# Performance work log

Hardware: AMD Instinct MI355X
Metric: run time of the kernel (lower is better)

The kernel has to match this reference:

```python
import jax, jax.numpy as jnp
import numpy as np

A, B, S, ADIM = 8, 8192, 128, 16   # n_agents, batch, state_dim, act_dim
H, HEADS = 512, 4                   # hidc, att_heads
D = H // HEADS                      # att_dim
EPS = 1e-5


def _ln(x):
    # LayerNorm over last dim, no affine (elementwise_affine=False), eps=1e-5
    m = jnp.mean(x, axis=-1, keepdims=True)
    v = jnp.var(x, axis=-1, keepdims=True)
    return (x - m) * jax.lax.rsqrt(v + EPS)


def setup_inputs() -> dict:
    key = jax.random.key(0)
    ks = jax.random.split(key, 16)
    sc = 0.02
    return {
        "states": jax.random.normal(ks[0], (A, B, S), jnp.float32),
        "actions": jax.random.normal(ks[1], (A, B, ADIM), jnp.float32),
        # per-agent state encoders (Encoder built with hidc in the source)
        "Ws_s": jax.random.normal(ks[2], (A, S, H), jnp.float32) * sc,
        "bs_s": jnp.zeros((A, H), jnp.float32),
        # per-agent state-action encoders
        "Ws_sa": jax.random.normal(ks[3], (A, S + ADIM, H), jnp.float32) * sc,
        "bs_sa": jnp.zeros((A, H), jnp.float32),
        # shared per-head key/value/selector projections
        "Wk": jax.random.normal(ks[4], (HEADS, H, D), jnp.float32) * sc,
        "Wv": jax.random.normal(ks[5], (HEADS, H, D), jnp.float32) * sc,
        "Wsel": jax.random.normal(ks[6], (HEADS, H, D), jnp.float32) * sc,
        "bsel": jnp.zeros((HEADS, D), jnp.float32),
        # per-agent critics: Linear(2H -> H), LeakyReLU, Linear(H -> ADIM)
        "Wc1": jax.random.normal(ks[7], (A, 2 * H, H), jnp.float32) * sc,
        "bc1": jnp.zeros((A, H), jnp.float32),
        "Wc2": jax.random.normal(ks[8], (A, H, ADIM), jnp.float32) * sc,
        "bc2": jnp.zeros((A, ADIM), jnp.float32),
    }


def reference(states, actions, Ws_s, bs_s, Ws_sa, bs_sa,
              Wk, Wv, Wsel, bsel, Wc1, bc1, Wc2, bc2):
    lrelu = jax.nn.leaky_relu  # slope 0.01 matches torch default

    # per-agent state encodings: [A,B,H]
    s_enc = lrelu(jnp.einsum('abs,ash->abh', _ln(states), Ws_s) + bs_s[:, None, :])

    # per-agent state-action encodings: [A,B,H]
    sa = jnp.concatenate([states, actions], axis=-1)
    sa_enc = lrelu(jnp.einsum('abs,ash->abh', _ln(sa), Ws_sa) + bs_sa[:, None, :])

    # per-head keys / values / selectors: [HEADS, A, B, D]
    keys = jnp.einsum('abh,khd->kabd', sa_enc, Wk)
    vals = jnp.einsum('abh,khd->kabd', sa_enc, Wv)
    sel = lrelu(jnp.einsum('abh,khd->kabd', sa_enc, Wsel) + bsel[:, None, None, :])

    # attention logits of agent i over agents j != i: [HEADS, A, A, B]
    logits = jnp.einsum('kibd,kjbd->kijb', sel, keys) / np.sqrt(D).astype(np.float32)
    self_mask = jnp.eye(A, dtype=bool)[None, :, :, None]
    w = jax.nn.softmax(jnp.where(self_mask, -jnp.inf, logits), axis=2)

    # attended values: [HEADS, A, B, D] -> concat heads -> [A, B, H]
    qvals = jnp.einsum('kijb,kjbd->kibd', w, vals)
    values = qvals.transpose(1, 2, 0, 3).reshape(A, B, H)

    # per-agent critics on concat(state_enc, attended values)
    cin = jnp.concatenate([s_enc, values], axis=-1)           # [A,B,2H]
    h1 = lrelu(jnp.einsum('abf,afh->abh', _ln(cin), Wc1) + bc1[:, None, :])
    all_qs = jnp.einsum('abh,aho->abo', h1, Wc2) + bc2[:, None, :]  # [A,B,ADIM]

    # Q of taken (argmax) action per agent: [A,B,1]
    idx = jnp.argmax(actions, axis=-1)
    q = jnp.take_along_axis(all_qs, idx[..., None], axis=-1)
    return q
```

## Files before the change

kernel.cpp:

```cpp
#include <hip/hip_runtime.h>
#include <hip/hip_bf16.h>
#include <math.h>


#define AN 8
#define BNB 8192
#define SN 128
#define ADN 16
#define HN 512
#define NHEADS 4
#define DN 128

typedef __hip_bfloat16 bf16;
typedef unsigned short u16;
typedef __attribute__((ext_vector_type(8))) short bf16x8;
typedef __attribute__((ext_vector_type(4))) float f32x4;

__device__ __forceinline__ float lrelu(float x){ return x > 0.f ? x : 0.01f*x; }
__device__ __forceinline__ float bflo(unsigned u){ return __uint_as_float(u << 16); }
__device__ __forceinline__ float bfhi(unsigned u){ return __uint_as_float(u & 0xffff0000u); }
__device__ __forceinline__ float bf2f(u16 u){ return __uint_as_float((unsigned)u << 16); }
__device__ __forceinline__ u16 f2bf(float v){
  union { bf16 h; u16 s; } cv; cv.h = __float2bfloat16(v); return cv.s;
}
__device__ __forceinline__ ushort4 f4bf(float4 v){
  ushort4 u; u.x=f2bf(v.x); u.y=f2bf(v.y); u.z=f2bf(v.z); u.w=f2bf(v.w); return u;
}

__device__ __forceinline__ void gload16(const u16* g, u16* l){
  __builtin_amdgcn_global_load_lds(
      (const __attribute__((address_space(1))) unsigned int*)(g),
      (__attribute__((address_space(3))) unsigned int*)(l), 16, 0, 0);
}

__global__ __launch_bounds__(256) void prep_kernel(
    const float* __restrict__ states, const float* __restrict__ actions,
    u16* __restrict__ sa_bf, float2* __restrict__ st_s, float2* __restrict__ st_sa,
    int* __restrict__ aip)
{
  const int lane = threadIdx.x & 63;
  const int r = blockIdx.x*4 + (threadIdx.x >> 6);
  float2 sv = ((const float2*)(states + (size_t)r*SN))[lane];
  float s1 = sv.x + sv.y, q1 = sv.x*sv.x + sv.y*sv.y;
  float2 av = make_float2(0.f, 0.f);
  if (lane < 8) av = ((const float2*)(actions + (size_t)r*ADN))[lane];
  float s2 = s1 + av.x + av.y, q2 = q1 + av.x*av.x + av.y*av.y;
  #pragma unroll
  for (int off=32; off; off>>=1){
    s1 += __shfl_xor(s1,off); q1 += __shfl_xor(q1,off);
    s2 += __shfl_xor(s2,off); q2 += __shfl_xor(q2,off);
  }
  float bv; int bi;
  if (lane < 8){
    if (av.x >= av.y){ bv = av.x; bi = 2*lane; } else { bv = av.y; bi = 2*lane+1; }
  } else { bv = -INFINITY; bi = 999; }
  #pragma unroll
  for (int off=1; off<8; off<<=1){
    float ov = __shfl_xor(bv, off); int oi = __shfl_xor(bi, off);
    if (ov > bv || (ov == bv && oi < bi)){ bv = ov; bi = oi; }
  }
  u16* row = sa_bf + (size_t)r*192;
  ushort2 p; p.x = f2bf(sv.x); p.y = f2bf(sv.y);
  *(ushort2*)(row + 2*lane) = p;
  if (lane < 8){
    ushort2 pa; pa.x = f2bf(av.x); pa.y = f2bf(av.y);
    *(ushort2*)(row + 128 + 2*lane) = pa;
  } else if (lane < 32){
    ushort2 z; z.x = 0; z.y = 0;
    *(ushort2*)(row + 128 + 2*lane) = z;
  }
  if (lane==0){
    float m1 = s1*(1.f/128.f), v1 = fmaxf(q1*(1.f/128.f)-m1*m1, 0.f);
    st_s[r] = make_float2(m1, rsqrtf(v1+1e-5f));
    float m2 = s2*(1.f/144.f), v2 = fmaxf(q2*(1.f/144.f)-m2*m2, 0.f);
    st_sa[r] = make_float2(m2, rsqrtf(v2+1e-5f));
    aip[r] = bi;
  }
}

__global__ __launch_bounds__(256) void transw_all_kernel(
    const float* __restrict__ Ws_s, const float* __restrict__ Ws_sa, const float* __restrict__ Wc1,
    const float* __restrict__ Wk, const float* __restrict__ Wv, const float* __restrict__ Wsel,
    u16* __restrict__ Wt_s, u16* __restrict__ Wt_sa, u16* __restrict__ Wt_c1, u16* __restrict__ Wt_p)
{
  __shared__ float t[32][33];
  int id = blockIdx.x;
  const float* in; u16* outp; int K, Kp; size_t zs; int gx;
  const int N = (id < 5376) ? 512 : 128;
  if (id < 512){            in=Ws_s;  outp=Wt_s;            K=128;  Kp=128;  zs=(size_t)512*128;  gx=4;  }
  else if (id < 1280){ id-=512;  in=Ws_sa; outp=Wt_sa;      K=144;  Kp=192;  zs=(size_t)512*192;  gx=6;  }
  else if (id < 5376){ id-=1280; in=Wc1;   outp=Wt_c1;      K=1024; Kp=1024; zs=(size_t)512*1024; gx=32; }
  else if (id < 5632){ id-=5376; in=Wk;    outp=Wt_p;            K=512; Kp=512; zs=(size_t)3*128*512; gx=16; }
  else if (id < 5888){ id-=5632; in=Wv;    outp=Wt_p+128*512;    K=512; Kp=512; zs=(size_t)3*128*512; gx=16; }
  else {               id-=5888; in=Wsel;  outp=Wt_p+2*128*512;  K=512; Kp=512; zs=(size_t)3*128*512; gx=16; }
  const int bx = id % gx; id /= gx;
  const int gy = N >> 5;
  const int by = id % gy;
  const int z  = id / gy;
  const int tx = threadIdx.x, ty = threadIdx.y;
  const int k0 = bx*32, n0 = by*32;
  const float* ip = in + (size_t)z*K*N;
  #pragma unroll
  for (int i=0;i<4;i++){
    int k = k0 + ty*4 + i;
    t[ty*4+i][tx] = (k < K) ? ip[(size_t)k*N + n0 + tx] : 0.f;
  }
  __syncthreads();
  u16* op = outp + (size_t)z*zs;
  #pragma unroll
  for (int i=0;i<4;i++){
    int n = n0 + ty*4 + i;
    op[(size_t)n*Kp + k0 + tx] = f2bf(t[tx][ty*4+i]);
  }
}

__global__ __launch_bounds__(256) void colsum_bf_kernel(
    const u16* __restrict__ Wt_s, const u16* __restrict__ Wt_sa, const u16* __restrict__ Wt_c1,
    float* __restrict__ cs_s, float* __restrict__ cs_sa, float* __restrict__ cs_c1)
{
  const int lane = threadIdx.x & 63;
  const int row = blockIdx.x*4 + (threadIdx.x >> 6);
  const int which = row >> 12; const int idx = row & 4095;
  const u16* W; int K; float* outp;
  if (which==0){ W = Wt_s;  K = 128;  outp = cs_s;  }
  else if (which==1){ W = Wt_sa; K = 192;  outp = cs_sa; }
  else { W = Wt_c1; K = 1024; outp = cs_c1; }
  const u16* p = W + (size_t)idx*K;
  float s = 0.f;
  for (int c = lane*8; c < K; c += 512){
    uint4 v = *(const uint4*)(p + c);
    const unsigned w4[4] = {v.x, v.y, v.z, v.w};
    #pragma unroll
    for (int t=0;t<4;t++) s += bflo(w4[t]) + bfhi(w4[t]);
  }
  #pragma unroll
  for (int off=32; off; off>>=1) s += __shfl_xor(s,off);
  if (lane==0) outp[idx] = s;
}

template<int MODE>
__global__ __launch_bounds__(256) void mfma_enc_kernel(
    const u16* __restrict__ Aa,
    const u16* __restrict__ Wt, const float* __restrict__ bias,
    const float2* __restrict__ stats, const float* __restrict__ csum,
    u16* __restrict__ outp)
{
  constexpr int K   = (MODE==0) ? 128 : 192;
  constexpr int LDA = 192;
  constexpr int KP  = K;
  __shared__ __align__(16) u16 smem[17408];
  u16* As = smem;
  u16* Bs = smem + 8192;
  const int tid = threadIdx.x;
  const int w = tid>>6, lane = tid&63;
  const int wr = w>>1, wc = w&1;
  const int srow = lane>>3, skq = (lane&7)^srow;

  const int nwg = gridDim.x * gridDim.y;
  int id = blockIdx.y * gridDim.x + blockIdx.x;
  int swz = (id & 7) * (nwg >> 3) + (id >> 3);
  const int bx = swz % gridDim.x, by = swz / gridDim.x;

  const int m0 = by*128, n0c = bx*128;
  const int a = by >> 6;
  const u16* Wbase = Wt + (size_t)a*HN*KP;
  const int slotbase = (lane>>4) ^ (lane&7);
  f32x4 acc[4][4] = {};

  for (int k0 = 0; k0 < K; k0 += 64){
    __syncthreads();
    #pragma unroll
    for (int t=0;t<4;t++){
      const int rr = w*32 + t*8;
      gload16(Aa    + (size_t)(m0  + rr + srow)*LDA + k0 + skq*8, As + rr*64);
      gload16(Wbase + (size_t)(n0c + rr + srow)*KP  + k0 + skq*8, Bs + rr*64);
    }
    __syncthreads();
    #pragma unroll
    for (int ks=0; ks<2; ++ks){
      bf16x8 af[4], bv[4];
      const int so = ((slotbase ^ (ks<<2)))*8;
      #pragma unroll
      for (int mi=0;mi<4;mi++) af[mi] = *(const bf16x8*)&As[(wr*64+mi*16+(lane&15))*64 + so];
      #pragma unroll
      for (int ni=0;ni<4;ni++) bv[ni] = *(const bf16x8*)&Bs[(wc*64+ni*16+(lane&15))*64 + so];
      #pragma unroll
      for (int mi=0;mi<4;mi++)
        #pragma unroll
        for (int ni=0;ni<4;ni++)
          acc[mi][ni] = __builtin_amdgcn_mfma_f32_16x16x32_bf16(af[mi], bv[ni], acc[mi][ni], 0, 0, 0);
    }
  }

  __syncthreads();
  float csv[4], biv[4];
  #pragma unroll
  for (int ni=0;ni<4;ni++){
    const int col = n0c + wc*64 + ni*16 + (lane&15);
    csv[ni] = csum[a*HN + col];
    biv[ni] = bias[a*HN + col];
  }
  #pragma unroll
  for (int mi=0;mi<4;mi++){
    const int rl = wr*64 + mi*16 + ((lane>>4)<<2);
    #pragma unroll
    for (int v=0; v<4; ++v){
      const float2 st = stats[m0 + rl + v];
      #pragma unroll
      for (int ni=0;ni<4;ni++){
        const float o = lrelu(st.y*(acc[mi][ni][v] - st.x*csv[ni]) + biv[ni]);
        smem[(rl+v)*136 + wc*64 + ni*16 + (lane&15)] = f2bf(o);
      }
    }
  }
  __syncthreads();
  #pragma unroll
  for (int it=0; it<8; ++it){
    const int rl = it*16 + (tid>>4);
    const int ck = (tid&15)*8;
    const uint4 vv = *(const uint4*)&smem[rl*136 + ck];
    *(uint4*)(outp + (size_t)(m0+rl)*HN + n0c + ck) = vv;
  }
}

__global__ __launch_bounds__(512, 2) void mfma_critic_kernel(
    const u16* __restrict__ Aa, const u16* __restrict__ Ab,
    const u16* __restrict__ Wt, const float* __restrict__ bias,
    const float2* __restrict__ stats, const float* __restrict__ csum,
    const float* __restrict__ Wc2, const float* __restrict__ bc2,
    const int* __restrict__ aip, float* __restrict__ qout)
{
  __shared__ __align__(16) u16 smem[74240];
  const int tid = threadIdx.x;
  const int w = tid >> 6, lane = tid & 63;
  const int wr = w >> 2, wc = w & 3;
  const int srow = lane >> 3, skq = (lane & 7) ^ srow;
  const int slotx = lane >> 4, lanx = lane & 7, lr = lane & 15;

  const int nwg = gridDim.x * gridDim.y;
  int id = blockIdx.y * gridDim.x + blockIdx.x;
  int swz = (id & 7) * (nwg >> 3) + (id >> 3);
  const int bx = swz % gridDim.x, by = swz / gridDim.x;
  const int m0 = by * 256, n0c = bx * 256;
  const int a = m0 >> 13;
  const u16* Wbase = Wt + (size_t)a * HN * 1024;

  float* wc2l = (float*)(smem + 65536);
  int*   ail  = (int*)(smem + 65536 + 8192);
  #pragma unroll
  for (int i = 0; i < 8; ++i){
    const int e = i*512 + tid;
    const int aidx = e >> 8, col = e & 255;
    wc2l[e] = Wc2[((size_t)a*HN + n0c + col)*ADN + aidx];
  }
  if (tid < 256) ail[tid] = aip[m0 + tid];

  auto STAGE = [&](int tau, int part){
    u16* dst = smem + (tau & 1)*32768 + ((part >> 1) ? 16384 : 0) + (part & 1)*8192 + w*1024;
    if (part < 2){
      const int k0 = tau * 64;
      const u16* asrc = (k0 < 512) ? Aa : Ab;
      const int acol = (k0 & 511) + skq*8;
      const int grow = m0 + (part & 1)*128 + w*16 + srow;
      gload16(asrc + (size_t)grow*HN + acol, dst);
      gload16(asrc + (size_t)(grow + 8)*HN + acol, dst + 512);
    } else {
      const int bcol = tau*64 + skq*8;
      const int grow = n0c + (part & 1)*128 + w*16 + srow;
      gload16(Wbase + (size_t)grow*1024 + bcol, dst);
      gload16(Wbase + (size_t)(grow + 8)*1024 + bcol, dst + 512);
    }
  };

  STAGE(0,0); STAGE(0,1); STAGE(0,2); STAGE(0,3);
  STAGE(1,0); STAGE(1,1); STAGE(1,2); STAGE(1,3);
  asm volatile("s_waitcnt vmcnt(8)" ::: "memory");
  __builtin_amdgcn_sched_barrier(0);
  __builtin_amdgcn_s_barrier();

  f32x4 acc[8][4] = {};

  #pragma unroll 1
  for (int tau = 0; tau < 16; ++tau){
    const u16* AB = smem + (tau & 1)*32768;
    const int so0 = ((0 | slotx) ^ lanx)*8;
    const int so1 = ((4 | slotx) ^ lanx)*8;
    bf16x8 af[4][2], bn01[2][2], bn23[2][2];

    #pragma unroll
    for (int mf = 0; mf < 4; ++mf){
      const int r = (wr*128 + mf*16 + lr)*64;
      af[mf][0] = *(const bf16x8*)&AB[r + so0];
      af[mf][1] = *(const bf16x8*)&AB[r + so1];
    }
    #pragma unroll
    for (int nf = 0; nf < 2; ++nf){
      const int r = 16384 + (wc*64 + nf*16 + lr)*64;
      bn01[nf][0] = *(const bf16x8*)&AB[r + so0];
      bn01[nf][1] = *(const bf16x8*)&AB[r + so1];
    }
    if (tau >= 1 && tau <= 14) STAGE(tau + 1, 0);
    __builtin_amdgcn_s_barrier();
    __builtin_amdgcn_s_setprio(1);
    #pragma unroll
    for (int mf = 0; mf < 4; ++mf)
      #pragma unroll
      for (int nf = 0; nf < 2; ++nf){
        acc[mf][nf] = __builtin_amdgcn_mfma_f32_16x16x32_bf16(af[mf][0], bn01[nf][0], acc[mf][nf], 0,0,0);
        acc[mf][nf] = __builtin_amdgcn_mfma_f32_16x16x32_bf16(af[mf][1], bn01[nf][1], acc[mf][nf], 0,0,0);
      }
    __builtin_amdgcn_s_setprio(0);
    __builtin_amdgcn_s_barrier();

    #pragma unroll
    for (int nf = 0; nf < 2; ++nf){
      const int r = 16384 + (wc*64 + (nf + 2)*16 + lr)*64;
      bn23[nf][0] = *(const bf16x8*)&AB[r + so0];
      bn23[nf][1] = *(const bf16x8*)&AB[r + so1];
    }
    if (tau >= 1 && tau <= 14) STAGE(tau + 1, 1);
    __builtin_amdgcn_s_barrier();
    __builtin_amdgcn_s_setprio(1);
    #pragma unroll
    for (int mf = 0; mf < 4; ++mf)
      #pragma unroll
      for (int nf = 0; nf < 2; ++nf){
        acc[mf][nf+2] = __builtin_amdgcn_mfma_f32_16x16x32_bf16(af[mf][0], bn23[nf][0], acc[mf][nf+2], 0,0,0);
        acc[mf][nf+2] = __builtin_amdgcn_mfma_f32_16x16x32_bf16(af[mf][1], bn23[nf][1], acc[mf][nf+2], 0,0,0);
      }
    __builtin_amdgcn_s_setprio(0);
    __builtin_amdgcn_s_barrier();

    #pragma unroll
    for (int mf = 0; mf < 4; ++mf){
      const int r = (wr*128 + (mf + 4)*16 + lr)*64;
      af[mf][0] = *(const bf16x8*)&AB[r + so0];
      af[mf][1] = *(const bf16x8*)&AB[r + so1];
    }
    if (tau <= 13) STAGE(tau + 2, 2);
    __builtin_amdgcn_s_barrier();
    __builtin_amdgcn_s_setprio(1);
    #pragma unroll
    for (int mf = 0; mf < 4; ++mf)
      #pragma unroll
      for (int nf = 0; nf < 2; ++nf){
        acc[mf+4][nf+2] = __builtin_amdgcn_mfma_f32_16x16x32_bf16(af[mf][0], bn23[nf][0], acc[mf+4][nf+2], 0,0,0);
        acc[mf+4][nf+2] = __builtin_amdgcn_mfma_f32_16x16x32_bf16(af[mf][1], bn23[nf][1], acc[mf+4][nf+2], 0,0,0);
      }
    __builtin_amdgcn_s_setprio(0);
    __builtin_amdgcn_s_barrier();

    if (tau <= 13) STAGE(tau + 2, 3);
    __builtin_amdgcn_s_barrier();
    __builtin_amdgcn_s_setprio(1);
    #pragma unroll
    for (int mf = 0; mf < 4; ++mf)
      #pragma unroll
      for (int nf = 0; nf < 2; ++nf){
        acc[mf+4][nf] = __builtin_amdgcn_mfma_f32_16x16x32_bf16(af[mf][0], bn01[nf][0], acc[mf+4][nf], 0,0,0);
        acc[mf+4][nf] = __builtin_amdgcn_mfma_f32_16x16x32_bf16(af[mf][1], bn01[nf][1], acc[mf+4][nf], 0,0,0);
      }
    __builtin_amdgcn_s_setprio(0);

    if (tau < 14)       { asm volatile("s_waitcnt vmcnt(4)" ::: "memory"); }
    else if (tau == 14) { asm volatile("s_waitcnt vmcnt(0)" ::: "memory"); }
    __builtin_amdgcn_sched_barrier(0);
    __builtin_amdgcn_s_barrier();
    __builtin_amdgcn_sched_barrier(0);
  }

  float csv[4], biv[4];
  #pragma unroll
  for (int nf = 0; nf < 4; ++nf){
    const int col = n0c + wc*64 + nf*16 + lr;
    csv[nf] = csum[a*HN + col];
    biv[nf] = bias[a*HN + col];
  }
  #pragma unroll
  for (int mf = 0; mf < 8; ++mf){
    const int rbase = wr*128 + mf*16 + slotx*4;
    #pragma unroll
    for (int v = 0; v < 4; ++v){
      const int rl = rbase + v;
      const float2 st = stats[m0 + rl];
      const int aidx = ail[rl];
      float p = 0.f;
      #pragma unroll
      for (int nf = 0; nf < 4; ++nf){
        const float o = lrelu(st.y*(acc[mf][nf][v] - st.x*csv[nf]) + biv[nf]);
        p = fmaf(o, wc2l[aidx*256 + wc*64 + nf*16 + lr], p);
      }
      p += __shfl_xor(p,1); p += __shfl_xor(p,2);
      p += __shfl_xor(p,4); p += __shfl_xor(p,8);
      if (lr == 0){
        if (n0c == 0 && wc == 0) p += bc2[a*ADN + aidx];
        atomicAdd(qout + m0 + rl, p);
      }
    }
  }
}

__global__ __launch_bounds__(256) void mfma_proj_kernel(
    const u16* __restrict__ sa_enc, const u16* __restrict__ Wt_p,
    const float* __restrict__ bsel, u16* __restrict__ kvs, int head)
{
  __shared__ __align__(16) u16 smem[17408];
  u16* As = smem;
  u16* Bs = smem + 8192;
  const int tid = threadIdx.x;
  const int w = tid>>6, lane = tid&63;
  const int wr = w>>1, wc = w&1;
  const int srow = lane>>3, skq = (lane&7)^srow;

  const int nwg = gridDim.x * gridDim.y;
  int id = blockIdx.y * gridDim.x + blockIdx.x;
  int swz = (id & 7) * (nwg >> 3) + (id >> 3);
  const int t = swz % gridDim.x;
  const int m0 = (swz / gridDim.x) * 128;

  const u16* Wbase = Wt_p + (size_t)(head*3 + t)*DN*HN;
  const int slotbase = (lane>>4) ^ (lane&7);
  f32x4 acc[4][4] = {};

  for (int k0 = 0; k0 < HN; k0 += 64){
    __syncthreads();
    #pragma unroll
    for (int tt=0;tt<4;tt++){
      const int rr = w*32 + tt*8;
      gload16(sa_enc + (size_t)(m0 + rr + srow)*HN + k0 + skq*8, As + rr*64);
      gload16(Wbase  + (size_t)(rr + srow)*HN      + k0 + skq*8, Bs + rr*64);
    }
    __syncthreads();
    #pragma unroll
    for (int ks=0; ks<2; ++ks){
      bf16x8 af[4], bv[4];
      const int so = ((slotbase ^ (ks<<2)))*8;
      #pragma unroll
      for (int mi=0;mi<4;mi++) af[mi] = *(const bf16x8*)&As[(wr*64+mi*16+(lane&15))*64 + so];
      #pragma unroll
      for (int ni=0;ni<4;ni++) bv[ni] = *(const bf16x8*)&Bs[(wc*64+ni*16+(lane&15))*64 + so];
      #pragma unroll
      for (int mi=0;mi<4;mi++)
        #pragma unroll
        for (int ni=0;ni<4;ni++)
          acc[mi][ni] = __builtin_amdgcn_mfma_f32_16x16x32_bf16(af[mi], bv[ni], acc[mi][ni], 0, 0, 0);
    }
  }

  __syncthreads();
  const bool issel = (t == 2);
  float biv[4];
  #pragma unroll
  for (int ni=0;ni<4;ni++){
    const int col = wc*64 + ni*16 + (lane&15);
    biv[ni] = issel ? bsel[head*DN + col] : 0.f;
  }
  #pragma unroll
  for (int mi=0;mi<4;mi++){
    const int rl = wr*64 + mi*16 + ((lane>>4)<<2);
    #pragma unroll
    for (int v=0; v<4; ++v){
      #pragma unroll
      for (int ni=0;ni<4;ni++){
        float o = acc[mi][ni][v] + biv[ni];
        if (issel) o = lrelu(o);
        smem[(rl+v)*136 + wc*64 + ni*16 + (lane&15)] = f2bf(o);
      }
    }
  }
  __syncthreads();
  #pragma unroll
  for (int it=0; it<8; ++it){
    const int rl = it*16 + (tid>>4);
    const int ck = (tid&15)*8;
    const int r = m0 + rl;
    const int ar = r >> 13, b = r & (BNB-1);
    const uint4 vv = *(const uint4*)&smem[rl*136 + ck];
    *(uint4*)(kvs + (((size_t)t*BNB + b)*AN + ar)*DN + ck) = vv;
  }
}

__global__ __launch_bounds__(256) void attn_kernel(
    const u16* __restrict__ kvs, u16* __restrict__ values, int kh)
{
  __shared__ float lds[4][3232];
  const int lane = threadIdx.x & 63;
  const int wv   = threadIdx.x >> 6;
  float* selL = &lds[wv][0];
  float* keyL = &lds[wv][1056];
  float* valL = &lds[wv][2112];
  float* wL   = &lds[wv][3168];
  const int b = blockIdx.x*4 + wv;

  #pragma unroll
  for (int m=0;m<3;m++){
    const int t = (m==0) ? 2 : ((m==1) ? 0 : 1);
    float* dst = (m==0) ? selL : ((m==1) ? keyL : valL);
    const uint2* p = (const uint2*)(kvs + ((size_t)t*BNB + b)*(AN*DN));
    #pragma unroll
    for (int it=0; it<4; it++){
      uint2 u = p[it*64 + lane];
      int e = (it*64 + lane)*4;
      int j = e >> 7, d = e & 127;
      float4 f;
      f.x = bflo(u.x); f.y = bfhi(u.x); f.z = bflo(u.y); f.w = bfhi(u.y);
      *(float4*)&dst[j*132 + d] = f;
    }
  }
  __syncthreads();

  const int i = lane >> 3, j = lane & 7;
  float acc = 0.f;
  #pragma unroll 8
  for (int dq=0; dq<32; dq++){
    const float4 s4 = *(const float4*)&selL[i*132 + dq*4];
    const float4 k4 = *(const float4*)&keyL[j*132 + dq*4];
    acc += s4.x*k4.x + s4.y*k4.y + s4.z*k4.z + s4.w*k4.w;
  }
  float logit = acc * 0.08838834764831845f;
  if (i == j) logit = -INFINITY;
  float mx = logit;
  mx = fmaxf(mx, __shfl_xor(mx,1,8));
  mx = fmaxf(mx, __shfl_xor(mx,2,8));
  mx = fmaxf(mx, __shfl_xor(mx,4,8));
  const float e = __expf(logit - mx);
  float s = e;
  s += __shfl_xor(s,1,8);
  s += __shfl_xor(s,2,8);
  s += __shfl_xor(s,4,8);
  wL[i*8 + j] = e / s;
  __syncthreads();

  const int dq = lane & 7;
  float4 o[4];
  #pragma unroll
  for (int tt=0;tt<4;tt++) o[tt] = make_float4(0.f,0.f,0.f,0.f);
  #pragma unroll
  for (int jj=0;jj<8;jj++){
    const float wj = wL[i*8 + jj];
    #pragma unroll
    for (int tt=0;tt<4;tt++){
      const float4 v4 = *(const float4*)&valL[jj*132 + tt*32 + dq*4];
      o[tt].x += wj*v4.x; o[tt].y += wj*v4.y; o[tt].z += wj*v4.z; o[tt].w += wj*v4.w;
    }
  }
  u16* dst = values + ((size_t)i*BNB + b)*HN + kh*DN;
  #pragma unroll
  for (int tt=0;tt<4;tt++)
    *(ushort4*)(dst + tt*32 + dq*4) = f4bf(o[tt]);
}

__global__ __launch_bounds__(256) void stats_cin_kernel(
    const u16* __restrict__ s_enc, const u16* __restrict__ values, float2* __restrict__ st)
{
  const int lane = threadIdx.x & 63;
  const int r = blockIdx.x*4 + (threadIdx.x >> 6);
  const uint4* p1 = (const uint4*)(s_enc + (size_t)r*HN);
  const uint4* p2 = (const uint4*)(values + (size_t)r*HN);
  uint4 va = p1[lane];
  uint4 vb = p2[lane];
  float s=0.f, q=0.f;
  const unsigned wa[4] = {va.x, va.y, va.z, va.w};
  const unsigned wb[4] = {vb.x, vb.y, vb.z, vb.w};
  #pragma unroll
  for (int t=0;t<4;t++){
    float f0 = bflo(wa[t]), f1 = bfhi(wa[t]);
    float g0 = bflo(wb[t]), g1 = bfhi(wb[t]);
    s += f0+f1+g0+g1; q += f0*f0+f1*f1+g0*g0+g1*g1;
  }
  #pragma unroll
  for (int off=32; off; off>>=1){ s += __shfl_xor(s,off); q += __shfl_xor(q,off); }
  if (lane==0){
    float m = s*(1.f/1024.f); float v = fmaxf(q*(1.f/1024.f) - m*m, 0.f);
    st[r] = make_float2(m, rsqrtf(v + 1e-5f));
  }
}

extern "C" void kernel_launch(void* const* d_in, const int* in_sizes, int n_in,
                              void* d_out, int out_size, void* d_ws, size_t ws_size,
                              hipStream_t stream)
{
  (void)in_sizes; (void)n_in; (void)ws_size;
  const float* states  = (const float*)d_in[0];
  const float* actions = (const float*)d_in[1];
  const float* Ws_s    = (const float*)d_in[2];
  const float* bs_s    = (const float*)d_in[3];
  const float* Ws_sa   = (const float*)d_in[4];
  const float* bs_sa   = (const float*)d_in[5];
  const float* Wk      = (const float*)d_in[6];
  const float* Wv      = (const float*)d_in[7];
  const float* Wsel    = (const float*)d_in[8];
  const float* bsel    = (const float*)d_in[9];
  const float* Wc1     = (const float*)d_in[10];
  const float* bc1     = (const float*)d_in[11];
  const float* Wc2     = (const float*)d_in[12];
  const float* bc2     = (const float*)d_in[13];
  float* outp = (float*)d_out;

  char* ws = (char*)d_ws;
  size_t off = 0;
  auto alloc = [&](size_t n){ void* p = ws + off; off += (n + 255) & ~(size_t)255; return p; };
  u16*    slot1  = (u16*)   alloc((size_t)AN*BNB*HN*2);
  u16*    s_enc  = slot1;
  u16*    kvs    = slot1;
  u16*    sa_enc = (u16*)   alloc((size_t)AN*BNB*HN*2);
  u16*    values = (u16*)   alloc((size_t)AN*BNB*HN*2);
  u16*    sa_bf  = (u16*)   alloc((size_t)AN*BNB*192*2);
  u16*    Wt_s   = (u16*)   alloc((size_t)AN*HN*128*2);
  u16*    Wt_sa  = (u16*)   alloc((size_t)AN*HN*192*2);
  u16*    Wt_c1  = (u16*)   alloc((size_t)AN*HN*1024*2);
  u16*    Wt_p   = (u16*)   alloc((size_t)NHEADS*3*DN*HN*2);
  float2* st_s   = (float2*)alloc((size_t)AN*BNB*8);
  float2* st_sa  = (float2*)alloc((size_t)AN*BNB*8);
  float2* st_cin = (float2*)alloc((size_t)AN*BNB*8);
  float*  cs_s   = (float*) alloc((size_t)AN*HN*4);
  float*  cs_sa  = (float*) alloc((size_t)AN*HN*4);
  float*  cs_c1  = (float*) alloc((size_t)AN*HN*4);
  int*    aip    = (int*)   alloc((size_t)AN*BNB*4);

  hipMemsetAsync(d_out, 0, (size_t)out_size*4, stream);
  prep_kernel<<<dim3(AN*BNB/4), 256, 0, stream>>>(states, actions, sa_bf, st_s, st_sa, aip);
  transw_all_kernel<<<dim3(6144), dim3(32,8), 0, stream>>>(
      Ws_s, Ws_sa, Wc1, Wk, Wv, Wsel, Wt_s, Wt_sa, Wt_c1, Wt_p);
  colsum_bf_kernel<<<dim3(3*AN*HN/4), 256, 0, stream>>>(Wt_s, Wt_sa, Wt_c1, cs_s, cs_sa, cs_c1);

  mfma_enc_kernel<1><<<dim3(4,512), 256, 0, stream>>>(sa_bf, Wt_sa, bs_sa, st_sa, cs_sa, sa_enc);
  for (int kh = 0; kh < NHEADS; ++kh){
    mfma_proj_kernel<<<dim3(3,512), 256, 0, stream>>>(sa_enc, Wt_p, bsel, kvs, kh);
    attn_kernel<<<dim3(BNB/4), 256, 0, stream>>>(kvs, values, kh);
  }
  mfma_enc_kernel<0><<<dim3(4,512), 256, 0, stream>>>(sa_bf, Wt_s, bs_s, st_s, cs_s, s_enc);
  stats_cin_kernel<<<dim3(AN*BNB/4), 256, 0, stream>>>(s_enc, values, st_cin);
  mfma_critic_kernel<<<dim3(2,256), 512, 0, stream>>>(s_enc, values, Wt_c1, bc1, st_cin, cs_c1,
                                                      Wc2, bc2, aip, outp);
}
```

Measured before the change: 460.9 us.

## Merge per-head projection and attention launches; keep attention tiles in bf16 LDS

When the workspace is large enough, the four per-head projection and attention launch pairs become one projection launch over all heads (12 column tiles) and one attention launch with a head grid dimension. This needs a larger key/value/selector buffer. The attention kernel now keeps sel/key/val in LDS as bf16 with an XOR swizzle instead of padded fp32. It drops the __syncthreads barriers, since each wave only touches its own tiles and gets softmax weights through shuffles, and it writes 16 outputs per lane as packed uint4. The aim is to cut launch count, improve occupancy through less LDS, and remove the barriers, at the cost of extra workspace and a dependence on the ws_size threshold.

```diff
diff --git a/kernel.cpp b/kernel.cpp
--- a/kernel.cpp
+++ b/kernel.cpp
@@ -23,8 +23,8 @@
 __device__ __forceinline__ u16 f2bf(float v){
   union { bf16 h; u16 s; } cv; cv.h = __float2bfloat16(v); return cv.s;
 }
-__device__ __forceinline__ ushort4 f4bf(float4 v){
-  ushort4 u; u.x=f2bf(v.x); u.y=f2bf(v.y); u.z=f2bf(v.z); u.w=f2bf(v.w); return u;
+__device__ __forceinline__ unsigned pk2(float a, float b){
+  return (unsigned)f2bf(a) | ((unsigned)f2bf(b) << 16);
 }
 
 __device__ __forceinline__ void gload16(const u16* g, u16* l){
@@ -402,7 +402,7 @@
 
 __global__ __launch_bounds__(256) void mfma_proj_kernel(
     const u16* __restrict__ sa_enc, const u16* __restrict__ Wt_p,
-    const float* __restrict__ bsel, u16* __restrict__ kvs, int head)
+    const float* __restrict__ bsel, u16* __restrict__ kvs, int head_or_m1)
 {
   __shared__ __align__(16) u16 smem[17408];
   u16* As = smem;
@@ -415,18 +415,21 @@
   const int nwg = gridDim.x * gridDim.y;
   int id = blockIdx.y * gridDim.x + blockIdx.x;
   int swz = (id & 7) * (nwg >> 3) + (id >> 3);
-  const int t = swz % gridDim.x;
+  const int tt = swz % gridDim.x;
   const int m0 = (swz / gridDim.x) * 128;
-
-  const u16* Wbase = Wt_p + (size_t)(head*3 + t)*DN*HN;
+  const int hw = (head_or_m1 >= 0) ? head_or_m1 : (tt / 3);
+  const int t  = (head_or_m1 >= 0) ? tt : (tt % 3);
+  u16* kvs_h = kvs + ((head_or_m1 >= 0) ? (size_t)0 : (size_t)hw * (3ull*BNB*AN*DN));
+
+  const u16* Wbase = Wt_p + (size_t)(hw*3 + t)*DN*HN;
   const int slotbase = (lane>>4) ^ (lane&7);
   f32x4 acc[4][4] = {};
 
   for (int k0 = 0; k0 < HN; k0 += 64){
     __syncthreads();
     #pragma unroll
-    for (int tt=0;tt<4;tt++){
-      const int rr = w*32 + tt*8;
+    for (int ttk=0;ttk<4;ttk++){
+      const int rr = w*32 + ttk*8;
       gload16(sa_enc + (size_t)(m0 + rr + srow)*HN + k0 + skq*8, As + rr*64);
       gload16(Wbase  + (size_t)(rr + srow)*HN      + k0 + skq*8, Bs + rr*64);
     }
@@ -453,7 +456,7 @@
   #pragma unroll
   for (int ni=0;ni<4;ni++){
     const int col = wc*64 + ni*16 + (lane&15);
-    biv[ni] = issel ? bsel[head*DN + col] : 0.f;
+    biv[ni] = issel ? bsel[hw*DN + col] : 0.f;
   }
   #pragma unroll
   for (int mi=0;mi<4;mi++){
@@ -476,78 +479,87 @@
     const int r = m0 + rl;
     const int ar = r >> 13, b = r & (BNB-1);
     const uint4 vv = *(const uint4*)&smem[rl*136 + ck];
-    *(uint4*)(kvs + (((size_t)t*BNB + b)*AN + ar)*DN + ck) = vv;
+    *(uint4*)(kvs_h + (((size_t)t*BNB + b)*AN + ar)*DN + ck) = vv;
   }
 }
 
 __global__ __launch_bounds__(256) void attn_kernel(
-    const u16* __restrict__ kvs, u16* __restrict__ values, int kh)
-{
-  __shared__ float lds[4][3232];
+    const u16* __restrict__ kvs, u16* __restrict__ values, int kh0, size_t kvstride)
+{
+  __shared__ u16 tiles[4][3][1024];
   const int lane = threadIdx.x & 63;
   const int wv   = threadIdx.x >> 6;
-  float* selL = &lds[wv][0];
-  float* keyL = &lds[wv][1056];
-  float* valL = &lds[wv][2112];
-  float* wL   = &lds[wv][3168];
+  const int head = kh0 + blockIdx.y;
   const int b = blockIdx.x*4 + wv;
-
-  #pragma unroll
-  for (int m=0;m<3;m++){
-    const int t = (m==0) ? 2 : ((m==1) ? 0 : 1);
-    float* dst = (m==0) ? selL : ((m==1) ? keyL : valL);
-    const uint2* p = (const uint2*)(kvs + ((size_t)t*BNB + b)*(AN*DN));
+  const u16* kb = kvs + (size_t)blockIdx.y * kvstride;
+
+  #pragma unroll
+  for (int t=0;t<3;t++){
+    const uint2* p = (const uint2*)(kb + ((size_t)t*BNB + b)*(AN*DN));
+    u16* dst = tiles[wv][t];
     #pragma unroll
     for (int it=0; it<4; it++){
-      uint2 u = p[it*64 + lane];
-      int e = (it*64 + lane)*4;
-      int j = e >> 7, d = e & 127;
-      float4 f;
-      f.x = bflo(u.x); f.y = bfhi(u.x); f.z = bflo(u.y); f.w = bfhi(u.y);
-      *(float4*)&dst[j*132 + d] = f;
-    }
-  }
-  __syncthreads();
+      const uint2 u = p[it*64 + lane];
+      const int e = (it*64 + lane)*4;
+      const int j = e >> 7, d = e & 127;
+      const int dsw = ((((d >> 3) ^ j) & 15) << 3) | (d & 7);
+      *(uint2*)&dst[j*128 + dsw] = u;
+    }
+  }
 
   const int i = lane >> 3, j = lane & 7;
-  float acc = 0.f;
-  #pragma unroll 8
-  for (int dq=0; dq<32; dq++){
-    const float4 s4 = *(const float4*)&selL[i*132 + dq*4];
-    const float4 k4 = *(const float4*)&keyL[j*132 + dq*4];
-    acc += s4.x*k4.x + s4.y*k4.y + s4.z*k4.z + s4.w*k4.w;
-  }
-  float logit = acc * 0.08838834764831845f;
+  const u16* selr = tiles[wv][2] + i*128;
+  const u16* keyr = tiles[wv][0] + j*128;
+  float dot = 0.f;
+  #pragma unroll
+  for (int c=0;c<16;c++){
+    const uint4 sv = *(const uint4*)&selr[((c ^ i) & 15) << 3];
+    const uint4 kv = *(const uint4*)&keyr[((c ^ j) & 15) << 3];
+    dot += bflo(sv.x)*bflo(kv.x) + bfhi(sv.x)*bfhi(kv.x);
+    dot += bflo(sv.y)*bflo(kv.y) + bfhi(sv.y)*bfhi(kv.y);
+    dot += bflo(sv.z)*bflo(kv.z) + bfhi(sv.z)*bfhi(kv.z);
+    dot += bflo(sv.w)*bflo(kv.w) + bfhi(sv.w)*bfhi(kv.w);
+  }
+  float logit = dot * 0.08838834764831845f;
   if (i == j) logit = -INFINITY;
   float mx = logit;
   mx = fmaxf(mx, __shfl_xor(mx,1,8));
   mx = fmaxf(mx, __shfl_xor(mx,2,8));
   mx = fmaxf(mx, __shfl_xor(mx,4,8));
   const float e = __expf(logit - mx);
-  float s = e;
-  s += __shfl_xor(s,1,8);
-  s += __shfl_xor(s,2,8);
-  s += __shfl_xor(s,4,8);
-  wL[i*8 + j] = e / s;
-  __syncthreads();
-
-  const int dq = lane & 7;
-  float4 o[4];
-  #pragma unroll
-  for (int tt=0;tt<4;tt++) o[tt] = make_float4(0.f,0.f,0.f,0.f);
-  #pragma unroll
-  for (int jj=0;jj<8;jj++){
-    const float wj = wL[i*8 + jj];
-    #pragma unroll
-    for (int tt=0;tt<4;tt++){
-      const float4 v4 = *(const float4*)&valL[jj*132 + tt*32 + dq*4];
-      o[tt].x += wj*v4.x; o[tt].y += wj*v4.y; o[tt].z += wj*v4.z; o[tt].w += wj*v4.w;
-    }
-  }
-  u16* dst = values + ((size_t)i*BNB + b)*HN + kh*DN;
-  #pragma unroll
-  for (int tt=0;tt<4;tt++)
-    *(ushort4*)(dst + tt*32 + dq*4) = f4bf(o[tt]);
+  float ssum = e;
+  ssum += __shfl_xor(ssum,1,8);
+  ssum += __shfl_xor(ssum,2,8);
+  ssum += __shfl_xor(ssum,4,8);
+  const float wgt = e / ssum;
+
+  const int dc = lane & 7;
+  float o[16];
+  #pragma unroll
+  for (int q = 0; q < 16; ++q) o[q] = 0.f;
+  #pragma unroll
+  for (int jj = 0; jj < 8; ++jj){
+    const float wj = __shfl(wgt, i*8 + jj);
+    const u16* valr = tiles[wv][1] + jj*128;
+    const uint4 v0 = *(const uint4*)&valr[(((2*dc)   ^ jj) & 15) << 3];
+    const uint4 v1 = *(const uint4*)&valr[(((2*dc+1) ^ jj) & 15) << 3];
+    o[0]  += wj*bflo(v0.x); o[1]  += wj*bfhi(v0.x);
+    o[2]  += wj*bflo(v0.y); o[3]  += wj*bfhi(v0.y);
+    o[4]  += wj*bflo(v0.z); o[5]  += wj*bfhi(v0.z);
+    o[6]  += wj*bflo(v0.w); o[7]  += wj*bfhi(v0.w);
+    o[8]  += wj*bflo(v1.x); o[9]  += wj*bfhi(v1.x);
+    o[10] += wj*bflo(v1.y); o[11] += wj*bfhi(v1.y);
+    o[12] += wj*bflo(v1.z); o[13] += wj*bfhi(v1.z);
+    o[14] += wj*bflo(v1.w); o[15] += wj*bfhi(v1.w);
+  }
+  uint4 p0, p1;
+  p0.x = pk2(o[0],o[1]);   p0.y = pk2(o[2],o[3]);
+  p0.z = pk2(o[4],o[5]);   p0.w = pk2(o[6],o[7]);
+  p1.x = pk2(o[8],o[9]);   p1.y = pk2(o[10],o[11]);
+  p1.z = pk2(o[12],o[13]); p1.w = pk2(o[14],o[15]);
+  u16* dst = values + ((size_t)i*BNB + b)*HN + head*DN + dc*16;
+  *(uint4*)dst = p0;
+  *(uint4*)(dst + 8) = p1;
 }
 
 __global__ __launch_bounds__(256) void stats_cin_kernel(
@@ -580,7 +592,7 @@
                               void* d_out, int out_size, void* d_ws, size_t ws_size,
                               hipStream_t stream)
 {
-  (void)in_sizes; (void)n_in; (void)ws_size;
+  (void)in_sizes; (void)n_in;
   const float* states  = (const float*)d_in[0];
   const float* actions = (const float*)d_in[1];
   const float* Ws_s    = (const float*)d_in[2];
@@ -597,12 +609,20 @@
   const float* bc2     = (const float*)d_in[13];
   float* outp = (float*)d_out;
 
+  const size_t KVH = (size_t)3*BNB*AN*DN;
+  const bool merged = ws_size >= (size_t)377*1024*1024;
+
   char* ws = (char*)d_ws;
   size_t off = 0;
   auto alloc = [&](size_t n){ void* p = ws + off; off += (n + 255) & ~(size_t)255; return p; };
-  u16*    slot1  = (u16*)   alloc((size_t)AN*BNB*HN*2);
-  u16*    s_enc  = slot1;
-  u16*    kvs    = slot1;
+  u16 *kvs, *s_enc;
+  if (merged){
+    kvs   = (u16*)alloc(KVH*NHEADS*2);
+    s_enc = kvs;
+  } else {
+    kvs   = (u16*)alloc((size_t)AN*BNB*HN*2);
+    s_enc = kvs;
+  }
   u16*    sa_enc = (u16*)   alloc((size_t)AN*BNB*HN*2);
   u16*    values = (u16*)   alloc((size_t)AN*BNB*HN*2);
   u16*    sa_bf  = (u16*)   alloc((size_t)AN*BNB*192*2);
@@ -625,9 +645,14 @@
   colsum_bf_kernel<<<dim3(3*AN*HN/4), 256, 0, stream>>>(Wt_s, Wt_sa, Wt_c1, cs_s, cs_sa, cs_c1);
 
   mfma_enc_kernel<1><<<dim3(4,512), 256, 0, stream>>>(sa_bf, Wt_sa, bs_sa, st_sa, cs_sa, sa_enc);
-  for (int kh = 0; kh < NHEADS; ++kh){
-    mfma_proj_kernel<<<dim3(3,512), 256, 0, stream>>>(sa_enc, Wt_p, bsel, kvs, kh);
-    attn_kernel<<<dim3(BNB/4), 256, 0, stream>>>(kvs, values, kh);
+  if (merged){
+    mfma_proj_kernel<<<dim3(12,512), 256, 0, stream>>>(sa_enc, Wt_p, bsel, kvs, -1);
+    attn_kernel<<<dim3(BNB/4, NHEADS), 256, 0, stream>>>(kvs, values, 0, KVH);
+  } else {
+    for (int kh = 0; kh < NHEADS; ++kh){
+      mfma_proj_kernel<<<dim3(3,512), 256, 0, stream>>>(sa_enc, Wt_p, bsel, kvs, kh);
+      attn_kernel<<<dim3(BNB/4, 1), 256, 0, stream>>>(kvs, values, kh, 0);
+    }
   }
   mfma_enc_kernel<0><<<dim3(4,512), 256, 0, stream>>>(sa_bf, Wt_s, bs_s, st_s, cs_s, s_enc);
   stats_cin_kernel<<<dim3(AN*BNB/4), 256, 0, stream>>>(s_enc, values, st_cin);
```

Measured after the change: 470.6 us. 1.02x slower.
